# Optimization experiments

Measured on AMD Instinct MI355X. Metric: run time of the kernel, lower is better.

Reference implementation:

```python
import jax, jax.numpy as jnp
import numpy as np

WS = 4           # window size (cubic)
NUM_HEADS = 4
DIM = 128
NW = 392         # number of windows per sample
B = 8            # batch
N = WS ** 3      # 64 tokens per window


def _relative_position_index(ws):
    coords = np.stack(np.meshgrid(np.arange(ws), np.arange(ws), np.arange(ws), indexing='ij'))  # [3,ws,ws,ws]
    flat = coords.reshape(3, -1)                      # [3, ws^3]
    rel = flat[:, :, None] - flat[:, None, :]         # [3, N, N]
    rel = rel.transpose(1, 2, 0).copy()               # [N, N, 3]
    rel += ws - 1
    rel[:, :, 0] *= (2 * ws - 1) ** 2
    rel[:, :, 1] *= (2 * ws - 1)
    return rel.sum(-1)                                # [N, N] int


def setup_inputs() -> dict:
    key = jax.random.key(0)
    ks = jax.random.split(key, 8)
    B_ = NW * B
    x = jax.random.normal(ks[0], (B_, N, DIM), dtype=jnp.float32)
    mask = jax.random.normal(ks[1], (NW, N, N), dtype=jnp.float32)
    # learned params
    qkv_w = jax.random.normal(ks[2], (3 * DIM, DIM), dtype=jnp.float32) * 0.02
    qkv_b = jnp.zeros((3 * DIM,), dtype=jnp.float32)
    proj_w = jax.random.normal(ks[3], (DIM, DIM), dtype=jnp.float32) * 0.02
    proj_b = jnp.zeros((DIM,), dtype=jnp.float32)
    tbl = jax.random.normal(ks[4], ((2 * WS - 1) ** 3, NUM_HEADS), dtype=jnp.float32) * 0.02
    rel_index = jnp.asarray(_relative_position_index(WS), dtype=jnp.int32)  # [N, N]
    return {"x": x, "mask": mask, "qkv_w": qkv_w, "qkv_b": qkv_b,
            "proj_w": proj_w, "proj_b": proj_b, "rpb_table": tbl,
            "rel_index": rel_index}


def reference(x, mask, qkv_w, qkv_b, proj_w, proj_b, rpb_table, rel_index):
    B_, N_, C = x.shape
    H = NUM_HEADS
    hd = C // H
    scale = hd ** (-0.5)
    # qkv projection: [B_, N, 3, H, hd] -> (3, B_, H, N, hd)
    qkv = (x @ qkv_w.T + qkv_b).reshape(B_, N_, 3, H, hd).transpose(2, 0, 3, 1, 4)
    q, k, v = qkv[0], qkv[1], qkv[2]
    attn = jnp.einsum('bhnd,bhmd->bhnm', q * scale, k)        # [B_, H, N, N]
    # gathered relative position bias: [N, N, H] -> [H, N, N]
    rpe = rpb_table[rel_index].transpose(2, 0, 1)
    attn = attn + rpe[None]
    nW = mask.shape[0]
    attn = attn.reshape(B_ // nW, nW, H, N_, N_) + mask[None, :, None]
    attn = attn.reshape(B_, H, N_, N_)
    attn = jax.nn.softmax(attn, axis=-1)
    out = jnp.einsum('bhnm,bhmd->bnhd', attn, v).reshape(B_, N_, C)
    return out @ proj_w.T + proj_b
```

## Files before the change

kernel.cpp:

```cpp
#include <hip/hip_runtime.h>
#include <hip/hip_bf16.h>


typedef __bf16 bf16x8 __attribute__((ext_vector_type(8)));
typedef __bf16 bf16x4 __attribute__((ext_vector_type(4)));
typedef float f32x4 __attribute__((ext_vector_type(4)));

#define NWMASK 392
#define SCALE 0.17677669529663687f

__global__ void prep(const float* __restrict__ qkv_w, const float* __restrict__ proj_w,
                     const float* __restrict__ tbl, const int* __restrict__ ridx,
                     __bf16* __restrict__ wqkv, __bf16* __restrict__ wproj,
                     float* __restrict__ rpe) {
    int i = blockIdx.x * 256 + threadIdx.x;
    if (i < 49152) {
        wqkv[i] = (__bf16)qkv_w[i];
    } else if (i < 65536) {
        int j = i - 49152;  wproj[j] = (__bf16)proj_w[j];
    } else {
        int j = i - 65536;
        rpe[j] = tbl[ridx[j & 4095] * 4 + (j >> 12)];
    }
}

__global__ __launch_bounds__(256, 4) void wattn_main(
    const float* __restrict__ x, const float* __restrict__ mask,
    const float* __restrict__ qkv_b, const float* __restrict__ proj_b,
    const __bf16* __restrict__ wqkv, const __bf16* __restrict__ wproj,
    const float* __restrict__ rpe, float* __restrict__ out)
{
    __shared__ __align__(16) __bf16 smem[18944];
    const int win  = blockIdx.x;
    const int tid  = threadIdx.x;
    const int h    = tid >> 6;
    const int lane = tid & 63;
    const int quad = lane >> 4;
    const int l16  = lane & 15;

    __bf16* const xs  = smem;
    __bf16* const buf = smem + 8704 + h * 2560;
    __bf16* const osw = smem + h * 2176;

    {
        const float* xb = x + (size_t)win * 8192;
        #pragma unroll
        for (int i = 0; i < 2; ++i) {
            const int row  = h * 16 + (lane >> 3) + i * 8;
            const int colg = (lane & 7) * 16;
            const float* xp = xb + row * 128 + colg;
            float4 a0 = *(const float4*)(xp);
            float4 a1 = *(const float4*)(xp + 4);
            float4 a2 = *(const float4*)(xp + 8);
            float4 a3 = *(const float4*)(xp + 12);
            bf16x8 t0, t1;
            t0[0]=(__bf16)a0.x; t0[1]=(__bf16)a0.y; t0[2]=(__bf16)a0.z; t0[3]=(__bf16)a0.w;
            t0[4]=(__bf16)a1.x; t0[5]=(__bf16)a1.y; t0[6]=(__bf16)a1.z; t0[7]=(__bf16)a1.w;
            t1[0]=(__bf16)a2.x; t1[1]=(__bf16)a2.y; t1[2]=(__bf16)a2.z; t1[3]=(__bf16)a2.w;
            t1[4]=(__bf16)a3.x; t1[5]=(__bf16)a3.y; t1[6]=(__bf16)a3.z; t1[7]=(__bf16)a3.w;
            *(bf16x8*)(xs + row * 136 + colg)     = t0;
            *(bf16x8*)(xs + row * 136 + colg + 8) = t1;
        }
    }
    __syncthreads();

    bf16x8 kf[4], qf[4], vf[2][2];

    {
        bf16x8 wf[2][4]; float bb[2];
        #pragma unroll
        for (int nt = 0; nt < 2; ++nt) {
            const int ng = 128 + h * 32 + nt * 16 + l16;
            bb[nt] = qkv_b[ng];
            #pragma unroll
            for (int kt = 0; kt < 4; ++kt)
                wf[nt][kt] = *(const bf16x8*)(wqkv + ng * 128 + kt * 32 + quad * 8);
        }
        #pragma unroll
        for (int mt = 0; mt < 4; ++mt) {
            bf16x8 af[4];
            #pragma unroll
            for (int kt = 0; kt < 4; ++kt)
                af[kt] = *(const bf16x8*)(xs + (mt * 16 + l16) * 136 + kt * 32 + quad * 8);
            #pragma unroll
            for (int nt = 0; nt < 2; ++nt) {
                f32x4 acc = {0.f, 0.f, 0.f, 0.f};
                #pragma unroll
                for (int kt = 0; kt < 4; ++kt)
                    acc = __builtin_amdgcn_mfma_f32_16x16x32_bf16(af[kt], wf[nt][kt], acc, 0, 0, 0);
                #pragma unroll
                for (int r = 0; r < 4; ++r)
                    buf[(mt * 16 + quad * 4 + r) * 40 + nt * 16 + l16] = (__bf16)(acc[r] + bb[nt]);
            }
        }
        #pragma unroll
        for (int j = 0; j < 4; ++j)
            kf[j] = *(const bf16x8*)(buf + (j * 16 + l16) * 40 + quad * 8);
    }

    {
        bf16x8 wf[2][4]; float bb[2];
        #pragma unroll
        for (int nt = 0; nt < 2; ++nt) {
            const int ng = h * 32 + nt * 16 + l16;
            bb[nt] = qkv_b[ng];
            #pragma unroll
            for (int kt = 0; kt < 4; ++kt)
                wf[nt][kt] = *(const bf16x8*)(wqkv + ng * 128 + kt * 32 + quad * 8);
        }
        #pragma unroll
        for (int mt = 0; mt < 4; ++mt) {
            bf16x8 af[4];
            #pragma unroll
            for (int kt = 0; kt < 4; ++kt)
                af[kt] = *(const bf16x8*)(xs + (mt * 16 + l16) * 136 + kt * 32 + quad * 8);
            #pragma unroll
            for (int nt = 0; nt < 2; ++nt) {
                f32x4 acc = {0.f, 0.f, 0.f, 0.f};
                #pragma unroll
                for (int kt = 0; kt < 4; ++kt)
                    acc = __builtin_amdgcn_mfma_f32_16x16x32_bf16(af[kt], wf[nt][kt], acc, 0, 0, 0);
                #pragma unroll
                for (int r = 0; r < 4; ++r)
                    buf[(mt * 16 + quad * 4 + r) * 40 + nt * 16 + l16] = (__bf16)((acc[r] + bb[nt]) * SCALE);
            }
        }
        #pragma unroll
        for (int mt = 0; mt < 4; ++mt)
            qf[mt] = *(const bf16x8*)(buf + (mt * 16 + l16) * 40 + quad * 8);
    }

    {
        bf16x8 wf[2][4]; float bb[2];
        #pragma unroll
        for (int nt = 0; nt < 2; ++nt) {
            const int ng = 256 + h * 32 + nt * 16 + l16;
            bb[nt] = qkv_b[ng];
            #pragma unroll
            for (int kt = 0; kt < 4; ++kt)
                wf[nt][kt] = *(const bf16x8*)(wqkv + ng * 128 + kt * 32 + quad * 8);
        }
        #pragma unroll
        for (int mt = 0; mt < 4; ++mt) {
            bf16x8 af[4];
            #pragma unroll
            for (int kt = 0; kt < 4; ++kt)
                af[kt] = *(const bf16x8*)(xs + (mt * 16 + l16) * 136 + kt * 32 + quad * 8);
            #pragma unroll
            for (int nt = 0; nt < 2; ++nt) {
                f32x4 acc = {0.f, 0.f, 0.f, 0.f};
                #pragma unroll
                for (int kt = 0; kt < 4; ++kt)
                    acc = __builtin_amdgcn_mfma_f32_16x16x32_bf16(af[kt], wf[nt][kt], acc, 0, 0, 0);
                bf16x4 pk;
                #pragma unroll
                for (int r = 0; r < 4; ++r) pk[r] = (__bf16)(acc[r] + bb[nt]);
                *(bf16x4*)(buf + (nt * 16 + l16) * 72 + mt * 16 + quad * 4) = pk;
            }
        }
        #pragma unroll
        for (int kt = 0; kt < 2; ++kt)
            #pragma unroll
            for (int nf = 0; nf < 2; ++nf)
                vf[kt][nf] = *(const bf16x8*)(buf + (nf * 16 + l16) * 72 + kt * 32 + quad * 8);
    }
    __syncthreads();

    const float* rpeh = rpe + h * 4096;
    const float* mw   = mask + (size_t)(win % NWMASK) * 4096;
    #pragma unroll
    for (int mt = 0; mt < 4; ++mt) {
        f32x4 sc[4];
        #pragma unroll
        for (int nt = 0; nt < 4; ++nt) {
            f32x4 z = {0.f, 0.f, 0.f, 0.f};
            sc[nt] = __builtin_amdgcn_mfma_f32_16x16x32_bf16(qf[mt], kf[nt], z, 0, 0, 0);
        }
        float inv_s[4];
        #pragma unroll
        for (int r = 0; r < 4; ++r) {
            const int row = mt * 16 + quad * 4 + r;
            float mx = -3.0e38f;
            #pragma unroll
            for (int nt = 0; nt < 4; ++nt) {
                float lg = sc[nt][r] + rpeh[row * 64 + nt * 16 + l16] + mw[row * 64 + nt * 16 + l16];
                sc[nt][r] = lg;
                mx = fmaxf(mx, lg);
            }
            #pragma unroll
            for (int s = 1; s < 16; s <<= 1) mx = fmaxf(mx, __shfl_xor(mx, s, 64));
            float sum = 0.f;
            #pragma unroll
            for (int nt = 0; nt < 4; ++nt) {
                float e = __expf(sc[nt][r] - mx);
                sc[nt][r] = e;
                sum += e;
            }
            #pragma unroll
            for (int s = 1; s < 16; s <<= 1) sum += __shfl_xor(sum, s, 64);
            inv_s[r] = 1.0f / sum;
        }
        #pragma unroll
        for (int nt = 0; nt < 4; ++nt)
            #pragma unroll
            for (int r = 0; r < 4; ++r)
                buf[(quad * 4 + r) * 72 + nt * 16 + l16] = (__bf16)sc[nt][r];
        f32x4 oa[2] = {{0.f,0.f,0.f,0.f},{0.f,0.f,0.f,0.f}};
        #pragma unroll
        for (int kt = 0; kt < 2; ++kt) {
            bf16x8 pf = *(const bf16x8*)(buf + l16 * 72 + kt * 32 + quad * 8);
            #pragma unroll
            for (int nf = 0; nf < 2; ++nf)
                oa[nf] = __builtin_amdgcn_mfma_f32_16x16x32_bf16(pf, vf[kt][nf], oa[nf], 0, 0, 0);
        }
        #pragma unroll
        for (int nf = 0; nf < 2; ++nf)
            #pragma unroll
            for (int r = 0; r < 4; ++r)
                osw[(mt * 16 + quad * 4 + r) * 34 + nf * 16 + l16] = (__bf16)(oa[nf][r] * inv_s[r]);
    }
    __syncthreads();

    bf16x8 of[4];
    #pragma unroll
    for (int kt = 0; kt < 4; ++kt)
        of[kt] = *(const bf16x8*)(smem + kt * 2176 + (h * 16 + l16) * 34 + quad * 8);
    #pragma unroll
    for (int nt = 0; nt < 8; ++nt) {
        const int ng = nt * 16 + l16;
        const float b = proj_b[ng];
        bf16x8 wf[4];
        #pragma unroll
        for (int kt = 0; kt < 4; ++kt)
            wf[kt] = *(const bf16x8*)(wproj + ng * 128 + kt * 32 + quad * 8);
        f32x4 acc = {0.f, 0.f, 0.f, 0.f};
        #pragma unroll
        for (int kt = 0; kt < 4; ++kt)
            acc = __builtin_amdgcn_mfma_f32_16x16x32_bf16(of[kt], wf[kt], acc, 0, 0, 0);
        float* dst = out + ((size_t)win * 64 + h * 16 + quad * 4) * 128 + ng;
        #pragma unroll
        for (int r = 0; r < 4; ++r) dst[(size_t)r * 128] = acc[r] + b;
    }
}

extern "C" void kernel_launch(void* const* d_in, const int* in_sizes, int n_in,
                              void* d_out, int out_size, void* d_ws, size_t ws_size,
                              hipStream_t stream) {
    const float* x      = (const float*)d_in[0];
    const float* mask   = (const float*)d_in[1];
    const float* qkv_w  = (const float*)d_in[2];
    const float* qkv_b  = (const float*)d_in[3];
    const float* proj_w = (const float*)d_in[4];
    const float* proj_b = (const float*)d_in[5];
    const float* tbl    = (const float*)d_in[6];
    const int*   ridx   = (const int*)d_in[7];
    float* out = (float*)d_out;

    __bf16* wqkv  = (__bf16*)d_ws;
    __bf16* wproj = wqkv + 384 * 128;
    float*  rpe   = (float*)((char*)d_ws + 131072);

    prep<<<320, 256, 0, stream>>>(qkv_w, proj_w, tbl, ridx, wqkv, wproj, rpe);
    wattn_main<<<3136, 256, 0, stream>>>(x, mask, qkv_b, proj_b, wqkv, wproj, rpe, out);
}
```

Before: 275.7 us.

## Precombine mask and bias in fragment order; drop softmax max; sum rows via MFMA

A new prep kernel adds the shifted-window mask and the gathered relative position bias into one fp32 tensor per mask window and head. It stores the values in MFMA accumulator order, so the main kernel can add them with one vector load per tile. The softmax no longer subtracts the row max, and the row sums come from an MFMA against a ones vector instead of cross-lane shuffle reductions. Launch bounds drop to 3 blocks per SM. The cost is an extra ~25 MB prep write on every call and more bias traffic per block, and skipping the max subtraction risks overflow for large logits.

```diff
diff --git a/kernel.cpp b/kernel.cpp
--- a/kernel.cpp
+++ b/kernel.cpp
@@ -24,11 +24,25 @@
     }
 }
 
-__global__ __launch_bounds__(256, 4) void wattn_main(
+__global__ void prep_cmb(const float* __restrict__ mask, const float* __restrict__ tbl,
+                         const int* __restrict__ ridx, float* __restrict__ cmb) {
+    int t = blockIdx.x * 256 + threadIdx.x;
+    int w = t >> 14;
+    int h = (t >> 12) & 3;
+    int j = t & 4095;
+    int mt = j >> 10, nt = (j >> 8) & 3, lane = (j >> 2) & 63, r = j & 3;
+    int row = mt * 16 + (lane >> 4) * 4 + r;
+    int col = nt * 16 + (lane & 15);
+    cmb[t] = mask[w * 4096 + row * 64 + col] + tbl[ridx[row * 64 + col] * 4 + h];
+}
+
+template<bool USE_CMB>
+__global__ __launch_bounds__(256, 3) void wattn_main(
     const float* __restrict__ x, const float* __restrict__ mask,
     const float* __restrict__ qkv_b, const float* __restrict__ proj_b,
     const __bf16* __restrict__ wqkv, const __bf16* __restrict__ wproj,
-    const float* __restrict__ rpe, float* __restrict__ out)
+    const float* __restrict__ rpe, const float* __restrict__ cmb,
+    float* __restrict__ out)
 {
     __shared__ __align__(16) __bf16 smem[18944];
     const int win  = blockIdx.x;
@@ -168,6 +182,10 @@
 
     const float* rpeh = rpe + h * 4096;
     const float* mw   = mask + (size_t)(win % NWMASK) * 4096;
+    const float* cbh  = cmb + (((size_t)(win % NWMASK) * 4 + h) << 12);
+    const __bf16 onev = (l16 == 0) ? (__bf16)1.0f : (__bf16)0.0f;
+    const bf16x8 ones = {onev, onev, onev, onev, onev, onev, onev, onev};
+
     #pragma unroll
     for (int mt = 0; mt < 4; ++mt) {
         f32x4 sc[4];
@@ -176,48 +194,43 @@
             f32x4 z = {0.f, 0.f, 0.f, 0.f};
             sc[nt] = __builtin_amdgcn_mfma_f32_16x16x32_bf16(qf[mt], kf[nt], z, 0, 0, 0);
         }
-        float inv_s[4];
+        if (USE_CMB) {
+            #pragma unroll
+            for (int nt = 0; nt < 4; ++nt)
+                sc[nt] += *(const f32x4*)(cbh + mt * 1024 + nt * 256 + lane * 4);
+        } else {
+            #pragma unroll
+            for (int nt = 0; nt < 4; ++nt)
+                #pragma unroll
+                for (int r = 0; r < 4; ++r) {
+                    const int row = mt * 16 + quad * 4 + r;
+                    sc[nt][r] += rpeh[row * 64 + nt * 16 + l16] + mw[row * 64 + nt * 16 + l16];
+                }
+        }
+        #pragma unroll
+        for (int nt = 0; nt < 4; ++nt)
+            #pragma unroll
+            for (int r = 0; r < 4; ++r) {
+                float e = __expf(sc[nt][r]);
+                buf[(quad * 4 + r) * 72 + nt * 16 + l16] = (__bf16)e;
+            }
+        bf16x8 pf0 = *(const bf16x8*)(buf + l16 * 72 + quad * 8);
+        bf16x8 pf1 = *(const bf16x8*)(buf + l16 * 72 + 32 + quad * 8);
+        f32x4 ss = {0.f, 0.f, 0.f, 0.f};
+        ss = __builtin_amdgcn_mfma_f32_16x16x32_bf16(pf0, ones, ss, 0, 0, 0);
+        ss = __builtin_amdgcn_mfma_f32_16x16x32_bf16(pf1, ones, ss, 0, 0, 0);
+        f32x4 oa0 = {0.f, 0.f, 0.f, 0.f}, oa1 = {0.f, 0.f, 0.f, 0.f};
+        oa0 = __builtin_amdgcn_mfma_f32_16x16x32_bf16(pf0, vf[0][0], oa0, 0, 0, 0);
+        oa0 = __builtin_amdgcn_mfma_f32_16x16x32_bf16(pf1, vf[1][0], oa0, 0, 0, 0);
+        oa1 = __builtin_amdgcn_mfma_f32_16x16x32_bf16(pf0, vf[0][1], oa1, 0, 0, 0);
+        oa1 = __builtin_amdgcn_mfma_f32_16x16x32_bf16(pf1, vf[1][1], oa1, 0, 0, 0);
         #pragma unroll
         for (int r = 0; r < 4; ++r) {
-            const int row = mt * 16 + quad * 4 + r;
-            float mx = -3.0e38f;
-            #pragma unroll
-            for (int nt = 0; nt < 4; ++nt) {
-                float lg = sc[nt][r] + rpeh[row * 64 + nt * 16 + l16] + mw[row * 64 + nt * 16 + l16];
-                sc[nt][r] = lg;
-                mx = fmaxf(mx, lg);
-            }
-            #pragma unroll
-            for (int s = 1; s < 16; s <<= 1) mx = fmaxf(mx, __shfl_xor(mx, s, 64));
-            float sum = 0.f;
-            #pragma unroll
-            for (int nt = 0; nt < 4; ++nt) {
-                float e = __expf(sc[nt][r] - mx);
-                sc[nt][r] = e;
-                sum += e;
-            }
-            #pragma unroll
-            for (int s = 1; s < 16; s <<= 1) sum += __shfl_xor(sum, s, 64);
-            inv_s[r] = 1.0f / sum;
-        }
-        #pragma unroll
-        for (int nt = 0; nt < 4; ++nt)
-            #pragma unroll
-            for (int r = 0; r < 4; ++r)
-                buf[(quad * 4 + r) * 72 + nt * 16 + l16] = (__bf16)sc[nt][r];
-        f32x4 oa[2] = {{0.f,0.f,0.f,0.f},{0.f,0.f,0.f,0.f}};
-        #pragma unroll
-        for (int kt = 0; kt < 2; ++kt) {
-            bf16x8 pf = *(const bf16x8*)(buf + l16 * 72 + kt * 32 + quad * 8);
-            #pragma unroll
-            for (int nf = 0; nf < 2; ++nf)
-                oa[nf] = __builtin_amdgcn_mfma_f32_16x16x32_bf16(pf, vf[kt][nf], oa[nf], 0, 0, 0);
-        }
-        #pragma unroll
-        for (int nf = 0; nf < 2; ++nf)
-            #pragma unroll
-            for (int r = 0; r < 4; ++r)
-                osw[(mt * 16 + quad * 4 + r) * 34 + nf * 16 + l16] = (__bf16)(oa[nf][r] * inv_s[r]);
+            const float s  = __shfl(ss[r], lane & 48, 64);
+            const float iv = 1.0f / s;
+            osw[(mt * 16 + quad * 4 + r) * 34 + l16]      = (__bf16)(oa0[r] * iv);
+            osw[(mt * 16 + quad * 4 + r) * 34 + 16 + l16] = (__bf16)(oa1[r] * iv);
+        }
     }
     __syncthreads();
 
@@ -259,7 +272,15 @@
     __bf16* wqkv  = (__bf16*)d_ws;
     __bf16* wproj = wqkv + 384 * 128;
     float*  rpe   = (float*)((char*)d_ws + 131072);
+    float*  cmb   = (float*)((char*)d_ws + 196608);
+    const size_t need_cmb = 196608 + (size_t)NWMASK * 4 * 4096 * 4;
+    const bool use_cmb = ws_size >= need_cmb;
 
     prep<<<320, 256, 0, stream>>>(qkv_w, proj_w, tbl, ridx, wqkv, wproj, rpe);
-    wattn_main<<<3136, 256, 0, stream>>>(x, mask, qkv_b, proj_b, wqkv, wproj, rpe, out);
-}
+    if (use_cmb) {
+        prep_cmb<<<25088, 256, 0, stream>>>(mask, tbl, ridx, cmb);
+        wattn_main<true><<<3136, 256, 0, stream>>>(x, mask, qkv_b, proj_b, wqkv, wproj, rpe, cmb, out);
+    } else {
+        wattn_main<false><<<3136, 256, 0, stream>>>(x, mask, qkv_b, proj_b, wqkv, wproj, rpe, cmb, out);
+    }
+}
```

New measurement: 288.2 us. +4.6%, slower.
